# Optimization experiments

Hardware: AMD Instinct MI355X
Metric: run time of the kernel (lower is better)

## Reference

```python
import jax, jax.numpy as jnp
import numpy as np

KH, KW = 7, 7
H, W = 4096, 4096

def setup_inputs() -> dict:
    key = jax.random.key(0)
    k1, k2 = jax.random.split(key)
    x = jax.random.normal(k1, (H, W), dtype=jnp.float32)
    weight = jax.random.normal(k2, (KH, KW), dtype=jnp.float32) * 0.001
    bias = jnp.zeros((1,), dtype=jnp.float32)
    return {"x": x, "weight": weight, "bias": bias}

def reference(x, weight, bias):
    # Single-channel valid 2D cross-correlation + scalar bias.
    # lax.conv_general_dilated performs cross-correlation (no kernel flip),
    # matching the torch loop: res[i,j] = sum(x[i:i+kh, j:j+kw] * k).
    lhs = x[None, None, :, :]            # [N=1, C=1, H, W]
    rhs = weight[None, None, :, :]       # [O=1, I=1, kh, kw]
    out = jax.lax.conv_general_dilated(
        lhs, rhs,
        window_strides=(1, 1),
        padding="VALID",
        dimension_numbers=("NCHW", "OIHW", "NCHW"),
    )
    return out[0, 0] + bias[0]           # [H-kh+1, W-kw+1]
```

## Files before the change

### kernel.cpp

```cpp
#include <hip/hip_runtime.h>
#include <stdint.h>

#define IH 4096
#define IW 4096
#define OH 4090
#define OW 4090

#define TW 256
#define TH 16
#define LW 272
#define LH 22
#define NV4 68
#define NLD (LH * NV4)
#define STEPS 4

typedef float v2f __attribute__((ext_vector_type(2)));
typedef __attribute__((address_space(1))) void gas_void;
typedef __attribute__((address_space(3))) void las_void;

__device__ __forceinline__ void stage_tile(const float* __restrict__ x,
                                           int tile_y0, int tile_x0,
                                           float* sbuf, int tid)
{
    const int wv = tid >> 6;
#pragma unroll
    for (int i = 0; i < (NLD + 255) / 256; ++i) {
        const int f = tid + i * 256;
        if (f < NLD) {
            const int r  = f / NV4;
            const int c4 = f - r * NV4;
            int iy = tile_y0 + r;
            iy = iy < IH ? iy : IH - 1;
            int c0 = tile_x0 + 4 * c4;
            c0 = c0 <= IW - 4 ? c0 : IW - 4;
            const float* gp = x + (size_t)iy * IW + c0;
            float* lp = sbuf + (size_t)(i * 256 + wv * 64) * 4;
            __builtin_amdgcn_global_load_lds((gas_void*)gp, (las_void*)lp, 16, 0, 0);
        }
    }
}

__global__ __launch_bounds__(256) void conv7x7_kernel(
    const float* __restrict__ x,
    const float* __restrict__ w,
    const float* __restrict__ bias,
    float* __restrict__ out)
{
    __shared__ float smem[2][LH * LW];

    const int tid     = threadIdx.x;
    const int tile_x0 = blockIdx.x * TW;
    const int ytile0  = blockIdx.y * STEPS;

    float wt[49];
#pragma unroll
    for (int k = 0; k < 49; ++k) wt[k] = w[k];
    const float b = bias[0];

    stage_tile(x, ytile0 * TH, tile_x0, smem[0], tid);

    const int tx  = tid & 63;
    const int wv  = tid >> 6;
    const int lx0 = 4 * tx;

    for (int s = 0; s < STEPS; ++s) {
        __syncthreads();
        if (s + 1 < STEPS)
            stage_tile(x, (ytile0 + s + 1) * TH, tile_x0, smem[(s + 1) & 1], tid);

        const float* sb = smem[s & 1];

        float acc[4][4];
#pragma unroll
        for (int r = 0; r < 4; ++r)
#pragma unroll
            for (int c = 0; c < 4; ++c) acc[r][c] = b;

#pragma unroll
        for (int ir = 0; ir < 10; ++ir) {
            const float* srow = sb + (4 * wv + ir) * LW + lx0;
            const float4 q0 = *(const float4*)(srow);
            const float4 q1 = *(const float4*)(srow + 4);
            const float4 q2 = *(const float4*)(srow + 8);
            float rb[12];
            rb[0]=q0.x; rb[1]=q0.y; rb[2]=q0.z;  rb[3]=q0.w;
            rb[4]=q1.x; rb[5]=q1.y; rb[6]=q1.z;  rb[7]=q1.w;
            rb[8]=q2.x; rb[9]=q2.y; rb[10]=q2.z; rb[11]=q2.w;

#pragma unroll
            for (int ky = 0; ky < 7; ++ky) {
                const int ry = ir - ky;
                if (ry >= 0 && ry < 4) {
#pragma unroll
                    for (int kx = 0; kx < 7; ++kx) {
                        const float wv_ = wt[ky * 7 + kx];
#pragma unroll
                        for (int c = 0; c < 4; ++c)
                            acc[ry][c] += wv_ * rb[kx + c];
                    }
                }
            }
        }

        const int ox0 = tile_x0 + lx0;
        const int oyb = (ytile0 + s) * TH + 4 * wv;
#pragma unroll
        for (int ry = 0; ry < 4; ++ry) {
            const int oy = oyb + ry;
            if (oy < OH) {
                float* orow = out + (size_t)oy * OW;
                if (ox0 + 3 < OW) {
                    v2f v0 = { acc[ry][0], acc[ry][1] };
                    v2f v1 = { acc[ry][2], acc[ry][3] };
                    __builtin_nontemporal_store(v0, (v2f*)(orow + ox0));
                    __builtin_nontemporal_store(v1, (v2f*)(orow + ox0 + 2));
                } else {
#pragma unroll
                    for (int c = 0; c < 4; ++c)
                        if (ox0 + c < OW) orow[ox0 + c] = acc[ry][c];
                }
            }
        }
    }
}

extern "C" void kernel_launch(void* const* d_in, const int* in_sizes, int n_in,
                              void* d_out, int out_size, void* d_ws, size_t ws_size,
                              hipStream_t stream) {
    const float* x    = (const float*)d_in[0];
    const float* w    = (const float*)d_in[1];
    const float* bias = (const float*)d_in[2];
    float* out        = (float*)d_out;

    dim3 grid((OW + TW - 1) / TW, (4096 / TH) / STEPS);
    conv7x7_kernel<<<grid, dim3(256), 0, stream>>>(x, w, bias, out);
}
```

Baseline: 130.2 us.

## Switch to 1024-thread blocks with taller row windows and 3x2 per-thread tiles

Changes the block to 1024 threads, each computing a 3x2 output patch, and streams 24-row steps with 30-row staged windows across 11 steps per block. The grid becomes 16x16 blocks, one per CU. The taller window is meant to cut halo reloading and give one large resident block per CU. In exchange, each output needs more LDS reads, per-thread register reuse drops, and the double-buffered LDS footprint grows.

```diff
diff --git a/kernel.cpp b/kernel.cpp
--- a/kernel.cpp
+++ b/kernel.cpp
@@ -7,118 +7,106 @@
 #define OW 4090
 
 #define TW 256
-#define TH 16
+#define STEP 24
+#define WIN 30
 #define LW 272
-#define LH 22
 #define NV4 68
-#define NLD (LH * NV4)
-#define STEPS 4
+#define NLD (WIN * NV4)
+#define NSTEPS 11
+#define BROWS (STEP * NSTEPS)
 
 typedef float v2f __attribute__((ext_vector_type(2)));
 typedef __attribute__((address_space(1))) void gas_void;
 typedef __attribute__((address_space(3))) void las_void;
 
 __device__ __forceinline__ void stage_tile(const float* __restrict__ x,
-                                           int tile_y0, int tile_x0,
-                                           float* sbuf, int tid)
+                                           int y0, int x0, float* sbuf,
+                                           int tid, int wv)
 {
-    const int wv = tid >> 6;
 #pragma unroll
-    for (int i = 0; i < (NLD + 255) / 256; ++i) {
-        const int f = tid + i * 256;
+    for (int i = 0; i < 2; ++i) {
+        const int f = tid + i * 1024;
         if (f < NLD) {
             const int r  = f / NV4;
             const int c4 = f - r * NV4;
-            int iy = tile_y0 + r;
+            int iy = y0 + r;
             iy = iy < IH ? iy : IH - 1;
-            int c0 = tile_x0 + 4 * c4;
+            int c0 = x0 + 4 * c4;
             c0 = c0 <= IW - 4 ? c0 : IW - 4;
             const float* gp = x + (size_t)iy * IW + c0;
-            float* lp = sbuf + (size_t)(i * 256 + wv * 64) * 4;
+            float* lp = sbuf + (size_t)(i * 1024 + wv * 64) * 4;
             __builtin_amdgcn_global_load_lds((gas_void*)gp, (las_void*)lp, 16, 0, 0);
         }
     }
 }
 
-__global__ __launch_bounds__(256) void conv7x7_kernel(
+__global__ __launch_bounds__(1024) void conv7x7_kernel(
     const float* __restrict__ x,
     const float* __restrict__ w,
     const float* __restrict__ bias,
     float* __restrict__ out)
 {
-    __shared__ float smem[2][LH * LW];
+    __shared__ float smem[2][WIN * LW];
 
-    const int tid     = threadIdx.x;
-    const int tile_x0 = blockIdx.x * TW;
-    const int ytile0  = blockIdx.y * STEPS;
+    const int tid = threadIdx.x;
+    const int wv  = tid >> 6;
+    const int txx = tid & 127;
+    const int tyy = tid >> 7;
+    const int x0  = blockIdx.x * TW;
+    const int yb  = blockIdx.y * BROWS;
 
     float wt[49];
 #pragma unroll
     for (int k = 0; k < 49; ++k) wt[k] = w[k];
     const float b = bias[0];
 
-    stage_tile(x, ytile0 * TH, tile_x0, smem[0], tid);
+    stage_tile(x, yb, x0, smem[0], tid, wv);
 
-    const int tx  = tid & 63;
-    const int wv  = tid >> 6;
-    const int lx0 = 4 * tx;
+    const int ox0 = x0 + 2 * txx;
 
-    for (int s = 0; s < STEPS; ++s) {
+    for (int s = 0; s < NSTEPS; ++s) {
         __syncthreads();
-        if (s + 1 < STEPS)
-            stage_tile(x, (ytile0 + s + 1) * TH, tile_x0, smem[(s + 1) & 1], tid);
+        if (s + 1 < NSTEPS)
+            stage_tile(x, yb + (s + 1) * STEP, x0, smem[(s + 1) & 1], tid, wv);
 
         const float* sb = smem[s & 1];
 
-        float acc[4][4];
+        float acc[3][2];
 #pragma unroll
-        for (int r = 0; r < 4; ++r)
-#pragma unroll
-            for (int c = 0; c < 4; ++c) acc[r][c] = b;
+        for (int r = 0; r < 3; ++r) { acc[r][0] = b; acc[r][1] = b; }
 
 #pragma unroll
-        for (int ir = 0; ir < 10; ++ir) {
-            const float* srow = sb + (4 * wv + ir) * LW + lx0;
-            const float4 q0 = *(const float4*)(srow);
-            const float4 q1 = *(const float4*)(srow + 4);
-            const float4 q2 = *(const float4*)(srow + 8);
-            float rb[12];
-            rb[0]=q0.x; rb[1]=q0.y; rb[2]=q0.z;  rb[3]=q0.w;
-            rb[4]=q1.x; rb[5]=q1.y; rb[6]=q1.z;  rb[7]=q1.w;
-            rb[8]=q2.x; rb[9]=q2.y; rb[10]=q2.z; rb[11]=q2.w;
+        for (int ir = 0; ir < 9; ++ir) {
+            const float* srow = sb + (3 * tyy + ir) * LW + 2 * txx;
+            float rb[8];
+            const float2 p0 = *(const float2*)(srow);
+            const float2 p1 = *(const float2*)(srow + 2);
+            const float2 p2 = *(const float2*)(srow + 4);
+            const float2 p3 = *(const float2*)(srow + 6);
+            rb[0]=p0.x; rb[1]=p0.y; rb[2]=p1.x; rb[3]=p1.y;
+            rb[4]=p2.x; rb[5]=p2.y; rb[6]=p3.x; rb[7]=p3.y;
 
 #pragma unroll
             for (int ky = 0; ky < 7; ++ky) {
                 const int ry = ir - ky;
-                if (ry >= 0 && ry < 4) {
+                if (ry >= 0 && ry < 3) {
 #pragma unroll
                     for (int kx = 0; kx < 7; ++kx) {
                         const float wv_ = wt[ky * 7 + kx];
-#pragma unroll
-                        for (int c = 0; c < 4; ++c)
-                            acc[ry][c] += wv_ * rb[kx + c];
+                        acc[ry][0] += wv_ * rb[kx];
+                        acc[ry][1] += wv_ * rb[kx + 1];
                     }
                 }
             }
         }
 
-        const int ox0 = tile_x0 + lx0;
-        const int oyb = (ytile0 + s) * TH + 4 * wv;
+        const int oyb = yb + s * STEP + 3 * tyy;
 #pragma unroll
-        for (int ry = 0; ry < 4; ++ry) {
+        for (int ry = 0; ry < 3; ++ry) {
             const int oy = oyb + ry;
-            if (oy < OH) {
-                float* orow = out + (size_t)oy * OW;
-                if (ox0 + 3 < OW) {
-                    v2f v0 = { acc[ry][0], acc[ry][1] };
-                    v2f v1 = { acc[ry][2], acc[ry][3] };
-                    __builtin_nontemporal_store(v0, (v2f*)(orow + ox0));
-                    __builtin_nontemporal_store(v1, (v2f*)(orow + ox0 + 2));
-                } else {
-#pragma unroll
-                    for (int c = 0; c < 4; ++c)
-                        if (ox0 + c < OW) orow[ox0 + c] = acc[ry][c];
-                }
+            if (oy < OH && ox0 < OW) {
+                v2f v = { acc[ry][0], acc[ry][1] };
+                __builtin_nontemporal_store(v, (v2f*)(out + (size_t)oy * OW + ox0));
             }
         }
     }
@@ -132,6 +120,6 @@
     const float* bias = (const float*)d_in[2];
     float* out        = (float*)d_out;
 
-    dim3 grid((OW + TW - 1) / TW, (4096 / TH) / STEPS);
-    conv7x7_kernel<<<grid, dim3(256), 0, stream>>>(x, w, bias, out);
+    dim3 grid(16, 16);
+    conv7x7_kernel<<<grid, dim3(1024), 0, stream>>>(x, w, bias, out);
 }
```

New measurement: 147.2 us. 1.13x slower.
